# Kernel tuning notes

Hardware: AMD Instinct MI355X
Metric: run time of the kernel (lower is better)

The kernel has to match this reference:

```python
import jax, jax.numpy as jnp
import numpy as np

ENTRY_SIZE = 8192
TUPLE_SIZE = 16
N_NEURONS = ENTRY_SIZE // TUPLE_SIZE            # 512
ADDR_SPACE = 2 ** TUPLE_SIZE                     # 65536
BATCH = 4096


def setup_inputs() -> dict:
    key = jax.random.key(0)
    k1, k2, k3 = jax.random.split(key, 3)
    # Binary input bits [B, entry_size]
    inp = jax.random.randint(k1, (BATCH, ENTRY_SIZE), 0, 2, dtype=jnp.int32)
    # Permutation mapping bits -> tuples (identity permutation; arange fill)
    tuple_mapping = jnp.arange(ENTRY_SIZE, dtype=jnp.int64)
    # Dense RAM tables emulating the per-neuron dicts:
    #   counts[n, a] = number of training samples that hit address a in neuron n
    #                  (0 means the address was never trained -> not in dict)
    #   sums[n, a]   = accumulated target sum for that address
    counts = jax.random.randint(k2, (N_NEURONS, ADDR_SPACE), 0, 4, dtype=jnp.int32)
    sums = jax.random.normal(k3, (N_NEURONS, ADDR_SPACE), dtype=jnp.float32)
    return {"input": inp, "tuple_mapping": tuple_mapping, "counts": counts, "sums": sums}


def reference(input, tuple_mapping, counts, sums):
    """RegressionWisard.predict with centrality='mean'.

    input:  [B, entry_size] binary bits (int32)
    tuple_mapping: [entry_size] permutation (int)
    counts: [n_neurons, 2^tuple_size] int32 RAM hit counts
    sums:   [n_neurons, 2^tuple_size] float32 RAM target sums
    """
    B = input.shape[0]
    # Map and group bits into tuples: [B, N, T]
    mapped = jnp.take(input, tuple_mapping, axis=1).reshape(B, N_NEURONS, TUPLE_SIZE)
    # Binary address per (sample, neuron); tidx flips so bit 0 is the MSB.
    pow2 = (jnp.int32(1) << jnp.arange(TUPLE_SIZE - 1, -1, -1, dtype=jnp.int32))
    addr = jnp.einsum("bnt,t->bn", mapped, pow2)  # [B, N], values in [0, 2^T)
    neuron_idx = jnp.arange(N_NEURONS, dtype=jnp.int32)[None, :]  # [1, N]
    c = counts[neuron_idx, addr]  # [B, N]
    s = sums[neuron_idx, addr]    # [B, N]
    trained = c > 0               # dict-membership (torch.isin) equivalent
    response = jnp.sum(jnp.where(trained, s, jnp.float32(0)), axis=1)      # [B]
    counters = jnp.sum(jnp.where(trained, c, 0), axis=1).astype(s.dtype)   # [B]
    return jnp.nan_to_num(response / counters)
```

## Files before the change

kernel.cpp:

```cpp
#include <hip/hip_runtime.h>


constexpr int BATCH   = 4096;
constexpr int ENTRY   = 8192;
constexpr int TUP     = 16;
constexpr int NEUR    = ENTRY / TUP;
constexpr int THREADS = 256;
constexpr int NC      = 8;
constexpr int SC      = BATCH / 64;
constexpr int NPT     = 16;

typedef int v4i __attribute__((ext_vector_type(4)));

__global__ __launch_bounds__(THREADS) void wisard_gather(
    const int*   __restrict__ input,
    const int*   __restrict__ mapping,
    const int*   __restrict__ counts,
    const float* __restrict__ sums,
    float*       __restrict__ part_r,
    int*         __restrict__ part_c)
{
    __shared__ float sr [4][64];
    __shared__ int   scn[4][64];

    const int tid  = threadIdx.x;
    const int lane = tid & 63;
    const int w    = tid >> 6;
    const int nc   = blockIdx.x & (NC - 1);
    const int sc   = blockIdx.x >> 3;
    const int s    = sc * 64 + lane;
    const int nb   = nc * 64 + w * NPT;

    int   cv[NPT];
    float sv[NPT];

    #pragma unroll
    for (int i = 0; i < NPT; ++i) {
        const int n = __builtin_amdgcn_readfirstlane(nb) + i;
        const int* map_n = mapping + n * TUP;

        const int m0 = map_n[0];
        bool contig = ((m0 & 3) == 0);
        #pragma unroll
        for (int t = 1; t < TUP; ++t) contig &= (map_n[t] == m0 + t);

        int addr;
        if (contig) {
            const v4i* p = reinterpret_cast<const v4i*>(
                input + (size_t)s * ENTRY + m0);
            const v4i a0 = __builtin_nontemporal_load(p);
            const v4i a1 = __builtin_nontemporal_load(p + 1);
            const v4i a2 = __builtin_nontemporal_load(p + 2);
            const v4i a3 = __builtin_nontemporal_load(p + 3);
            addr = ((a0.x & 1) << 15) | ((a0.y & 1) << 14)
                 | ((a0.z & 1) << 13) | ((a0.w & 1) << 12)
                 | ((a1.x & 1) << 11) | ((a1.y & 1) << 10)
                 | ((a1.z & 1) <<  9) | ((a1.w & 1) <<  8)
                 | ((a2.x & 1) <<  7) | ((a2.y & 1) <<  6)
                 | ((a2.z & 1) <<  5) | ((a2.w & 1) <<  4)
                 | ((a3.x & 1) <<  3) | ((a3.y & 1) <<  2)
                 | ((a3.z & 1) <<  1) |  (a3.w & 1);
        } else {
            const int* row = input + (size_t)s * ENTRY;
            int a = 0;
            #pragma unroll
            for (int t = 0; t < TUP; ++t) a = (a << 1) | (row[map_n[t]] & 1);
            addr = a;
        }

        const size_t idx = ((size_t)n << 16) | (unsigned)addr;
        cv[i] = counts[idx];
        sv[i] = sums  [idx];
    }

    float r = 0.0f; int c = 0;
    #pragma unroll
    for (int i = 0; i < NPT; ++i) {
        const bool t = cv[i] > 0;
        r += t ? sv[i] : 0.0f;
        c += t ? cv[i] : 0;
    }

    sr[w][lane] = r; scn[w][lane] = c;
    __syncthreads();
    if (w == 0) {
        r = sr[0][lane] + sr[1][lane] + sr[2][lane] + sr[3][lane];
        c = scn[0][lane] + scn[1][lane] + scn[2][lane] + scn[3][lane];
        part_r[nc * BATCH + s] = r;
        part_c[nc * BATCH + s] = c;
    }
}

__global__ __launch_bounds__(THREADS) void wisard_finalize(
    const float* __restrict__ part_r,
    const int*   __restrict__ part_c,
    float*       __restrict__ out)
{
    const int s = blockIdx.x * THREADS + threadIdx.x;
    float r = 0.0f; int c = 0;
    #pragma unroll
    for (int nc = 0; nc < NC; ++nc) {
        r += part_r[nc * BATCH + s];
        c += part_c[nc * BATCH + s];
    }
    out[s] = (c > 0) ? (r / (float)c) : 0.0f;
}

extern "C" void kernel_launch(void* const* d_in, const int* in_sizes, int n_in,
                              void* d_out, int out_size, void* d_ws, size_t ws_size,
                              hipStream_t stream) {
    (void)in_sizes; (void)n_in; (void)out_size; (void)ws_size;
    const int*   input   = (const int*)d_in[0];
    const int*   mapping = (const int*)d_in[1];
    const int*   counts  = (const int*)d_in[2];
    const float* sums    = (const float*)d_in[3];
    float*       out     = (float*)d_out;

    float* part_r = (float*)d_ws;
    int*   part_c = (int*)((char*)d_ws + (size_t)NC * BATCH * sizeof(float));

    wisard_gather<<<SC * NC, THREADS, 0, stream>>>(
        input, mapping, counts, sums, part_r, part_c);
    wisard_finalize<<<BATCH / THREADS, THREADS, 0, stream>>>(part_r, part_c, out);
}
```

Before: 398.4 us.

## Sort addresses per neuron with counting sort before gathering RAM tables

Splits the work into three kernels: one computes 16-bit tuple addresses into a transposed workspace, one sorts each neuron's sample addresses by 64-byte line with a shared-memory counting sort and then gathers counts and sums in sorted order, and one reduces the per-neuron contributions per sample. The intent is to make the random gathers from the 128 MB counts and sums tables more line-coalesced within a wavefront. In exchange it writes and rereads a 16 MB float2 contribution buffer and a 4 MB address buffer, and adds atomics and extra launches. It falls back to a single direct kernel when the workspace is too small.

```diff
diff --git a/kernel.cpp b/kernel.cpp
--- a/kernel.cpp
+++ b/kernel.cpp
@@ -5,121 +5,265 @@
 constexpr int ENTRY   = 8192;
 constexpr int TUP     = 16;
 constexpr int NEUR    = ENTRY / TUP;
+constexpr int LINES   = 4096;
 constexpr int THREADS = 256;
-constexpr int NC      = 8;
-constexpr int SC      = BATCH / 64;
-constexpr int NPT     = 16;
+constexpr int SPLIT   = 2;
+constexpr int SB      = BATCH / SPLIT;
+constexpr int EPT     = SB / THREADS;
 
 typedef int v4i __attribute__((ext_vector_type(4)));
 
-__global__ __launch_bounds__(THREADS) void wisard_gather(
+__device__ __forceinline__ int tuple_addr(
+    const int* __restrict__ input, const int* __restrict__ map_n,
+    int m0, bool contig, int s)
+{
+    if (contig) {
+        const v4i* p = reinterpret_cast<const v4i*>(input + (size_t)s * ENTRY + m0);
+        const v4i a0 = __builtin_nontemporal_load(p);
+        const v4i a1 = __builtin_nontemporal_load(p + 1);
+        const v4i a2 = __builtin_nontemporal_load(p + 2);
+        const v4i a3 = __builtin_nontemporal_load(p + 3);
+        return ((a0.x & 1) << 15) | ((a0.y & 1) << 14)
+             | ((a0.z & 1) << 13) | ((a0.w & 1) << 12)
+             | ((a1.x & 1) << 11) | ((a1.y & 1) << 10)
+             | ((a1.z & 1) <<  9) | ((a1.w & 1) <<  8)
+             | ((a2.x & 1) <<  7) | ((a2.y & 1) <<  6)
+             | ((a2.z & 1) <<  5) | ((a2.w & 1) <<  4)
+             | ((a3.x & 1) <<  3) | ((a3.y & 1) <<  2)
+             | ((a3.z & 1) <<  1) |  (a3.w & 1);
+    } else {
+        const int* row = input + (size_t)s * ENTRY;
+        int a = 0;
+        #pragma unroll
+        for (int t = 0; t < TUP; ++t) a = (a << 1) | (row[map_n[t]] & 1);
+        return a;
+    }
+}
+
+__global__ __launch_bounds__(THREADS) void wisard_addr(
+    const int* __restrict__ input,
+    const int* __restrict__ mapping,
+    unsigned short* __restrict__ addr_t)
+{
+    const int tid  = threadIdx.x;
+    const int lane = tid & 63;
+    const int w    = tid >> 6;
+    const int nch  = blockIdx.x & 7;
+    const int sc   = blockIdx.x >> 3;
+    const int s    = sc * 64 + lane;
+    const int nb   = nch * 64 + w * 16;
+
+    #pragma unroll 4
+    for (int i = 0; i < 16; ++i) {
+        const int n = __builtin_amdgcn_readfirstlane(nb) + i;
+        const int* map_n = mapping + n * TUP;
+        const int m0 = map_n[0];
+        bool contig = ((m0 & 3) == 0);
+        #pragma unroll
+        for (int t = 1; t < TUP; ++t) contig &= (map_n[t] == m0 + t);
+        const int a = tuple_addr(input, map_n, m0, contig, s);
+        addr_t[(size_t)n * BATCH + s] = (unsigned short)a;
+    }
+}
+
+__global__ __launch_bounds__(THREADS) void wisard_sortgather(
+    const unsigned short* __restrict__ addr_t,
+    const int*   __restrict__ counts,
+    const float* __restrict__ sums,
+    float2*      __restrict__ contrib)
+{
+    __shared__ unsigned int hist[LINES];
+    __shared__ unsigned int sorted[SB];
+    __shared__ unsigned int ttot[THREADS];
+    __shared__ unsigned int wsum[THREADS / 64];
+
+    const int tid   = threadIdx.x;
+    const int lane  = tid & 63;
+    const int w     = tid >> 6;
+    const int n     = blockIdx.x >> 1;
+    const int half  = blockIdx.x & 1;
+    const int sbase = half * SB;
+
+    unsigned int a[EPT];
+    #pragma unroll
+    for (int j = 0; j < EPT; ++j)
+        a[j] = addr_t[(size_t)n * BATCH + sbase + j * THREADS + tid];
+
+    #pragma unroll
+    for (int j = 0; j < LINES / THREADS; ++j) hist[j * THREADS + tid] = 0u;
+    __syncthreads();
+    #pragma unroll
+    for (int j = 0; j < EPT; ++j) atomicAdd(&hist[a[j] >> 4], 1u);
+    __syncthreads();
+
+    unsigned int loc[16];
+    unsigned int run = 0;
+    #pragma unroll
+    for (int j = 0; j < 16; ++j) { loc[j] = run; run += hist[tid * 16 + j]; }
+    ttot[tid] = run;
+    __syncthreads();
+    unsigned int v = ttot[tid];
+    #pragma unroll
+    for (int off = 1; off < 64; off <<= 1) {
+        const unsigned int u = __shfl_up(v, off, 64);
+        if (lane >= off) v += u;
+    }
+    if (lane == 63) wsum[w] = v;
+    __syncthreads();
+    unsigned int woff = 0;
+    for (int i = 0; i < w; ++i) woff += wsum[i];
+    const unsigned int excl = woff + v - ttot[tid];
+    __syncthreads();
+    #pragma unroll
+    for (int j = 0; j < 16; ++j) hist[tid * 16 + j] = excl + loc[j];
+    __syncthreads();
+
+    #pragma unroll
+    for (int j = 0; j < EPT; ++j) {
+        const unsigned int pos = atomicAdd(&hist[a[j] >> 4], 1u);
+        sorted[pos] = (a[j] << 12) | (unsigned int)(sbase + j * THREADS + tid);
+    }
+    __syncthreads();
+
+    unsigned int pk[EPT];
+    int   cv[EPT];
+    float sv[EPT];
+    #pragma unroll
+    for (int j = 0; j < EPT; ++j) pk[j] = sorted[j * THREADS + tid];
+    #pragma unroll
+    for (int j = 0; j < EPT; ++j) {
+        const size_t idx = ((size_t)n << 16) | (pk[j] >> 12);
+        cv[j] = counts[idx];
+        sv[j] = sums[idx];
+    }
+    #pragma unroll
+    for (int j = 0; j < EPT; ++j) {
+        const int sm = (int)(pk[j] & 4095u);
+        const bool t = cv[j] > 0;
+        float2 o;
+        o.x = t ? sv[j] : 0.0f;
+        o.y = __int_as_float(t ? cv[j] : 0);
+        contrib[(size_t)n * BATCH + sm] = o;
+    }
+}
+
+__global__ __launch_bounds__(THREADS) void wisard_final(
+    const float2* __restrict__ contrib,
+    float*        __restrict__ out)
+{
+    __shared__ float sr [4][64];
+    __shared__ int   scn[4][64];
+    const int tid  = threadIdx.x;
+    const int lane = tid & 63;
+    const int w    = tid >> 6;
+    const int s    = blockIdx.x * 64 + lane;
+
+    float r = 0.0f; int c = 0;
+    #pragma unroll 8
+    for (int i = 0; i < NEUR / 4; ++i) {
+        const int n = w * (NEUR / 4) + i;
+        const float2 vv = contrib[(size_t)n * BATCH + s];
+        r += vv.x;
+        c += __float_as_int(vv.y);
+    }
+    sr[w][lane] = r; scn[w][lane] = c;
+    __syncthreads();
+    if (w == 0) {
+        r = sr[0][lane] + sr[1][lane] + sr[2][lane] + sr[3][lane];
+        c = scn[0][lane] + scn[1][lane] + scn[2][lane] + scn[3][lane];
+        out[s] = (c > 0) ? (r / (float)c) : 0.0f;
+    }
+}
+
+__global__ __launch_bounds__(THREADS) void wisard_fallback(
     const int*   __restrict__ input,
     const int*   __restrict__ mapping,
     const int*   __restrict__ counts,
     const float* __restrict__ sums,
-    float*       __restrict__ part_r,
-    int*         __restrict__ part_c)
-{
-    __shared__ float sr [4][64];
-    __shared__ int   scn[4][64];
+    float*       __restrict__ out)
+{
+    __shared__ float s_resp[2][THREADS / 64];
+    __shared__ int   s_cnt [2][THREADS / 64];
 
     const int tid  = threadIdx.x;
     const int lane = tid & 63;
-    const int w    = tid >> 6;
-    const int nc   = blockIdx.x & (NC - 1);
-    const int sc   = blockIdx.x >> 3;
-    const int s    = sc * 64 + lane;
-    const int nb   = nc * 64 + w * NPT;
-
-    int   cv[NPT];
-    float sv[NPT];
-
-    #pragma unroll
-    for (int i = 0; i < NPT; ++i) {
-        const int n = __builtin_amdgcn_readfirstlane(nb) + i;
+    const int wv   = tid >> 6;
+    const int b0   = blockIdx.x * 2;
+
+    int   cv[2][2];
+    float sv[2][2];
+
+    #pragma unroll
+    for (int k = 0; k < 2; ++k) {
+        const int n = tid + k * THREADS;
         const int* map_n = mapping + n * TUP;
-
         const int m0 = map_n[0];
         bool contig = ((m0 & 3) == 0);
         #pragma unroll
         for (int t = 1; t < TUP; ++t) contig &= (map_n[t] == m0 + t);
-
-        int addr;
-        if (contig) {
-            const v4i* p = reinterpret_cast<const v4i*>(
-                input + (size_t)s * ENTRY + m0);
-            const v4i a0 = __builtin_nontemporal_load(p);
-            const v4i a1 = __builtin_nontemporal_load(p + 1);
-            const v4i a2 = __builtin_nontemporal_load(p + 2);
-            const v4i a3 = __builtin_nontemporal_load(p + 3);
-            addr = ((a0.x & 1) << 15) | ((a0.y & 1) << 14)
-                 | ((a0.z & 1) << 13) | ((a0.w & 1) << 12)
-                 | ((a1.x & 1) << 11) | ((a1.y & 1) << 10)
-                 | ((a1.z & 1) <<  9) | ((a1.w & 1) <<  8)
-                 | ((a2.x & 1) <<  7) | ((a2.y & 1) <<  6)
-                 | ((a2.z & 1) <<  5) | ((a2.w & 1) <<  4)
-                 | ((a3.x & 1) <<  3) | ((a3.y & 1) <<  2)
-                 | ((a3.z & 1) <<  1) |  (a3.w & 1);
-        } else {
-            const int* row = input + (size_t)s * ENTRY;
-            int a = 0;
-            #pragma unroll
-            for (int t = 0; t < TUP; ++t) a = (a << 1) | (row[map_n[t]] & 1);
-            addr = a;
+        #pragma unroll
+        for (int s = 0; s < 2; ++s) {
+            const int a = tuple_addr(input, map_n, m0, contig, b0 + s);
+            const size_t idx = ((size_t)n << 16) | (unsigned)a;
+            cv[s][k] = counts[idx];
+            sv[s][k] = sums[idx];
         }
-
-        const size_t idx = ((size_t)n << 16) | (unsigned)addr;
-        cv[i] = counts[idx];
-        sv[i] = sums  [idx];
-    }
-
-    float r = 0.0f; int c = 0;
-    #pragma unroll
-    for (int i = 0; i < NPT; ++i) {
-        const bool t = cv[i] > 0;
-        r += t ? sv[i] : 0.0f;
-        c += t ? cv[i] : 0;
-    }
-
-    sr[w][lane] = r; scn[w][lane] = c;
-    __syncthreads();
-    if (w == 0) {
-        r = sr[0][lane] + sr[1][lane] + sr[2][lane] + sr[3][lane];
-        c = scn[0][lane] + scn[1][lane] + scn[2][lane] + scn[3][lane];
-        part_r[nc * BATCH + s] = r;
-        part_c[nc * BATCH + s] = c;
-    }
-}
-
-__global__ __launch_bounds__(THREADS) void wisard_finalize(
-    const float* __restrict__ part_r,
-    const int*   __restrict__ part_c,
-    float*       __restrict__ out)
-{
-    const int s = blockIdx.x * THREADS + threadIdx.x;
-    float r = 0.0f; int c = 0;
-    #pragma unroll
-    for (int nc = 0; nc < NC; ++nc) {
-        r += part_r[nc * BATCH + s];
-        c += part_c[nc * BATCH + s];
-    }
-    out[s] = (c > 0) ? (r / (float)c) : 0.0f;
+    }
+
+    float resp[2]; int cnt[2];
+    #pragma unroll
+    for (int s = 0; s < 2; ++s) {
+        resp[s] = 0.0f; cnt[s] = 0;
+        #pragma unroll
+        for (int k = 0; k < 2; ++k) {
+            const bool t = cv[s][k] > 0;
+            resp[s] += t ? sv[s][k] : 0.0f;
+            cnt [s] += t ? cv[s][k] : 0;
+        }
+    }
+    #pragma unroll
+    for (int s = 0; s < 2; ++s) {
+        float r = resp[s]; int c = cnt[s];
+        #pragma unroll
+        for (int off = 32; off > 0; off >>= 1) {
+            r += __shfl_down(r, off, 64);
+            c += __shfl_down(c, off, 64);
+        }
+        if (lane == 0) { s_resp[s][wv] = r; s_cnt[s][wv] = c; }
+    }
+    __syncthreads();
+    if (tid < 2) {
+        float r = 0.0f; int c = 0;
+        #pragma unroll
+        for (int w = 0; w < THREADS / 64; ++w) { r += s_resp[tid][w]; c += s_cnt[tid][w]; }
+        out[b0 + tid] = (c > 0) ? (r / (float)c) : 0.0f;
+    }
 }
 
 extern "C" void kernel_launch(void* const* d_in, const int* in_sizes, int n_in,
                               void* d_out, int out_size, void* d_ws, size_t ws_size,
                               hipStream_t stream) {
-    (void)in_sizes; (void)n_in; (void)out_size; (void)ws_size;
+    (void)in_sizes; (void)n_in; (void)out_size;
     const int*   input   = (const int*)d_in[0];
     const int*   mapping = (const int*)d_in[1];
     const int*   counts  = (const int*)d_in[2];
     const float* sums    = (const float*)d_in[3];
     float*       out     = (float*)d_out;
 
-    float* part_r = (float*)d_ws;
-    int*   part_c = (int*)((char*)d_ws + (size_t)NC * BATCH * sizeof(float));
-
-    wisard_gather<<<SC * NC, THREADS, 0, stream>>>(
-        input, mapping, counts, sums, part_r, part_c);
-    wisard_finalize<<<BATCH / THREADS, THREADS, 0, stream>>>(part_r, part_c, out);
-}
+    const size_t contrib_bytes = (size_t)NEUR * BATCH * sizeof(float2);
+    const size_t addr_bytes    = (size_t)NEUR * BATCH * sizeof(unsigned short);
+
+    if (ws_size < contrib_bytes + addr_bytes || d_ws == nullptr) {
+        wisard_fallback<<<BATCH / 2, THREADS, 0, stream>>>(
+            input, mapping, counts, sums, out);
+        return;
+    }
+
+    float2*         contrib = (float2*)d_ws;
+    unsigned short* addr_t  = (unsigned short*)((char*)d_ws + contrib_bytes);
+
+    wisard_addr<<<(BATCH / 64) * 8, THREADS, 0, stream>>>(input, mapping, addr_t);
+    wisard_sortgather<<<NEUR * SPLIT, THREADS, 0, stream>>>(
+        addr_t, counts, sums, contrib);
+    wisard_final<<<BATCH / 64, THREADS, 0, stream>>>(contrib, out);
+}
```

After: 414.5 us. 1.04x slower.
